# Kernel optimization log

Measured on AMD Instinct MI355X. Metric: run time of the kernel, lower is better.

The kernel has to match this reference:

```python
import jax, jax.numpy as jnp
import numpy as np
from jax import lax

K2 = 3                 # support_kernel_size
TARGET_OCC = 0.5
OCC_W = 10.0
ITERS = 10             # flood-fill iterations
THRESH = 0.5
STEEP = 20.0

# 6-neighbor 3D cross kernel (plus-shaped), shape [O=1, I=1, 3, 3, 3]
_cross_np = np.zeros((1, 1, 3, 3, 3), dtype=np.float32)
for dz, dy, dx in [(0, 1, 1), (2, 1, 1), (1, 0, 1), (1, 2, 1), (1, 1, 0), (1, 1, 2)]:
    _cross_np[0, 0, dz, dy, dx] = 1.0


def _conv3d(x, k, pad):
    # x: [B, C, D, H, W], k: [O, I, kd, kh, kw]
    return lax.conv_general_dilated(
        x, k, window_strides=(1, 1, 1), padding=pad,
        dimension_numbers=('NCDHW', 'OIDHW', 'NCDHW'))


def setup_inputs() -> dict:
    key = jax.random.key(0)
    voxel_grid = jax.random.uniform(key, (4, 1, 128, 128, 128), dtype=jnp.float32)
    return {"voxel_grid": voxel_grid}


def reference(voxel_grid):
    B, C, D, H, W = voxel_grid.shape
    N = B * D * H * W
    dt = voxel_grid.dtype

    # ---- overhang score: vectorized over all z-slices at once ----
    # per-slice conv2d(3x3 ones) == conv3d with kernel depth 1
    k2 = jnp.ones((1, 1, 1, K2, K2), dt)
    below = voxel_grid[:, :, :-1]          # [B,1,D-1,H,W]
    curr = voxel_grid[:, :, 1:]
    below_support = _conv3d(below, k2, ((0, 0), (1, 1), (1, 1)))
    support_ratio = below_support / (K2 * K2)
    overhang = (curr * (1.0 - support_ratio)).sum() / N

    # ---- surface area score ----
    k3 = jnp.ones((1, 1, 3, 3, 3), dt)
    neighbor_solid = _conv3d(voxel_grid, k3, ((1, 1), (1, 1), (1, 1)))
    surface_term = neighbor_solid.sum() / 27.0 / N

    occupancy = voxel_grid.sum() / N
    occupancy_penalty = OCC_W * (occupancy - TARGET_OCC) ** 2

    # differentiable flood-fill (diff_find_enclosed_voids)
    seed = jnp.zeros_like(voxel_grid).at[:, :, 5, 5, 5].set(1.0)
    cross = jnp.asarray(_cross_np, dt)
    not_solid = 1.0 - voxel_grid

    def body(i, mask):
        c = _conv3d(mask, cross, ((1, 1), (1, 1), (1, 1)))
        act = jax.nn.sigmoid(STEEP * (c - THRESH))
        return jnp.maximum(mask, act) * not_solid

    enclosed = lax.fori_loop(0, ITERS, body, seed)
    resin_trap_penalty = 100.0 * enclosed.sum() / N

    surface_score = surface_term - resin_trap_penalty - occupancy_penalty
    return overhang, surface_score
```

## Files before the change

### kernel.cpp

```cpp
#include <hip/hip_runtime.h>

#define HW    (128*128)
#define DHW   (128*128*128)
#define NTOT  (4*DHW)
#define NBLK  2048

__device__ __forceinline__ float sigf(float x){ return 1.0f/(1.0f+__expf(-x)); }
__device__ __forceinline__ float4 ld4(const float* p){ return *(const float4*)p; }


__global__ __launch_bounds__(256, 4) void mega_k(
    const float* __restrict__ v, float* __restrict__ p_occ,
    float* __restrict__ p_surf, float* __restrict__ p_over,
    float* __restrict__ p_trap)
{
    __shared__ float4 smem4[1445];
    __shared__ float sred[16];
    float* smem = (float*)smem4;

    const int bid = blockIdx.x;
    const int tid = threadIdx.x;
    const float4 zero4 = make_float4(0,0,0,0);

    if (bid < 4) {
        const int b = bid;
        const size_t gb = (size_t)b * DHW;
        const int ty = tid & 15, tz = tid >> 4;
        const float a_lo = sigf(-10.0f), a_hi = sigf(10.0f);
        #define M(zz,yy) (smem + (((zz)*17 + (yy))*20))

        float m[16], nv[16];
        {
            const float* rv = v + gb + ((size_t)tz*128 + ty)*128;
            int dzy = abs(tz-5) + abs(ty-5);
            #pragma unroll
            for (int q = 0; q < 4; ++q) {
                int x4 = 4*q;
                float4 a = ld4(rv + x4);
                nv[x4+0]=1.f-a.x; nv[x4+1]=1.f-a.y; nv[x4+2]=1.f-a.z; nv[x4+3]=1.f-a.w;
                int d0=dzy+abs(x4+0-5), d1=dzy+abs(x4+1-5);
                int d2=dzy+abs(x4+2-5), d3=dzy+abs(x4+3-5);
                m[x4+0] = ((d0==0)?1.f:((d0==1)?a_hi:a_lo)) * nv[x4+0];
                m[x4+1] = ((d1==0)?1.f:((d1==1)?a_hi:a_lo)) * nv[x4+1];
                m[x4+2] = ((d2==0)?1.f:((d2==1)?a_hi:a_lo)) * nv[x4+2];
                m[x4+3] = ((d3==0)?1.f:((d3==1)?a_hi:a_lo)) * nv[x4+3];
                *(float4*)(M(tz,ty) + x4) = make_float4(m[x4+0],m[x4+1],m[x4+2],m[x4+3]);
            }
        }
        const float xrE = a_lo * (1.f - v[gb + ((size_t)tz*128 + ty)*128 + 16]);
        {
            int a = tid >> 4, e = tid & 15;
            M(16,a)[e] = a_lo * (1.f - v[gb + ((size_t)16*128 + a)*128 + e]);
            M(a,16)[e] = a_lo * (1.f - v[gb + ((size_t)a*128 + 16)*128 + e]);
        }
        __syncthreads();

        for (int it = 0; it < 9; ++it) {
            const float* YM = M(tz,ty-1);
            const float* YP = M(tz,ty+1);
            const float* ZM = M(tz-1,ty);
            const float* ZP = M(tz+1,ty);
            float nm[16];
            #pragma unroll
            for (int q = 0; q < 4; ++q) {
                int x4 = 4*q;
                float4 ym = (ty > 0) ? *(const float4*)(YM + x4) : zero4;
                float4 yp = *(const float4*)(YP + x4);
                float4 zm = (tz > 0) ? *(const float4*)(ZM + x4) : zero4;
                float4 zp = *(const float4*)(ZP + x4);
                float xl = (q == 0) ? 0.f : m[x4-1];
                float xr = (q == 3) ? xrE : m[x4+4];
                float s0 = xl      + m[x4+1] + ym.x + yp.x + zm.x + zp.x;
                float s1 = m[x4+0] + m[x4+2] + ym.y + yp.y + zm.y + zp.y;
                float s2 = m[x4+1] + m[x4+3] + ym.z + yp.z + zm.z + zp.z;
                float s3 = m[x4+2] + xr      + ym.w + yp.w + zm.w + zp.w;
                nm[x4+0] = fmaxf(m[x4+0], sigf(20.f*s0 - 10.f)) * nv[x4+0];
                nm[x4+1] = fmaxf(m[x4+1], sigf(20.f*s1 - 10.f)) * nv[x4+1];
                nm[x4+2] = fmaxf(m[x4+2], sigf(20.f*s2 - 10.f)) * nv[x4+2];
                nm[x4+3] = fmaxf(m[x4+3], sigf(20.f*s3 - 10.f)) * nv[x4+3];
            }
            __syncthreads();
            float* W = M(tz,ty);
            #pragma unroll
            for (int q = 0; q < 4; ++q) {
                int x4 = 4*q;
                *(float4*)(W + x4) = make_float4(nm[x4+0],nm[x4+1],nm[x4+2],nm[x4+3]);
                m[x4+0]=nm[x4+0]; m[x4+1]=nm[x4+1]; m[x4+2]=nm[x4+2]; m[x4+3]=nm[x4+3];
            }
            __syncthreads();
        }

        float d = 0.f;
        #pragma unroll
        for (int x = 0; x < 16; ++x) d += m[x] - a_lo * nv[x];
        #pragma unroll
        for (int o = 32; o; o >>= 1) d += __shfl_down(d, o, 64);
        int lane = tid & 63, wid = tid >> 6;
        if (lane == 0) sred[wid] = d;
        __syncthreads();
        if (tid == 0) p_trap[b] = sred[0] + sred[1] + sred[2] + sred[3];
        #undef M
    } else {
        const int rid = bid - 4;
        const int b   = rid >> 9;
        const int rem = rid & 511;
        const int z0  = (rem >> 4) * 4;
        const int y0  = (rem & 15) * 8;
        const int tx  = tid & 31, ty = tid >> 5;
        const int x4  = tx * 4;
        const int y   = y0 + ty;
        const size_t gb = (size_t)b * DHW;
        #define PB(p,r) (smem + ((p)*1320 + (r)*132))

        float occ = 0.f, surf = 0.f, over = 0.f;

        if (z0 >= 1) {
            const float* bp = v + gb + (size_t)(z0-1)*HW;
            for (int i = tid; i < 320; i += 256) {
                int r = i >> 5, xq = i & 31, xi = xq*4;
                int gy = y0 - 1 + r;
                float4 q = ((unsigned)gy <= 127u) ? ld4(bp + gy*128 + xi) : zero4;
                float ql = __shfl_up(q.w, 1);   if (xq == 0)  ql = 0.f;
                float qr = __shfl_down(q.x, 1); if (xq == 31) qr = 0.f;
                *(float4*)(PB(0,r) + xi) =
                    make_float4(ql+q.x+q.y, q.x+q.y+q.z, q.y+q.z+q.w, q.z+q.w+qr);
            }
        }
        __syncthreads();

        const float wy = (y==0 || y==127) ? 2.f : 3.f;
        const float wx0 = (x4==0)   ? 2.f : 3.f;
        const float wx3 = (x4==124) ? 2.f : 3.f;
        const float inv9 = 1.f/9.f;

        int pb = 0;
        for (int s = 0; s < 4; ++s) {
            const int z = z0 + s;
            const float* cp = v + gb + (size_t)z*HW;
            float4 val = ld4(cp + y*128 + x4);

            occ += val.x + val.y + val.z + val.w;
            float wz = (z==0 || z==127) ? 2.f : 3.f;
            surf += wz*wy*(wx0*val.x + 3.f*val.y + 3.f*val.z + wx3*val.w);

            if (z >= 1) {
                float4 a = *(const float4*)(PB(pb, ty)   + x4);
                float4 c = *(const float4*)(PB(pb, ty+1) + x4);
                float4 d = *(const float4*)(PB(pb, ty+2) + x4);
                float4 S = make_float4(a.x+c.x+d.x, a.y+c.y+d.y,
                                       a.z+c.z+d.z, a.w+c.w+d.w);
                over += val.x*(1.f - S.x*inv9) + val.y*(1.f - S.y*inv9)
                      + val.z*(1.f - S.z*inv9) + val.w*(1.f - S.w*inv9);
            }

            if (s < 3) {
                float ql = __shfl_up(val.w, 1);   if (tx == 0)  ql = 0.f;
                float qr = __shfl_down(val.x, 1); if (tx == 31) qr = 0.f;
                *(float4*)(PB(pb^1, ty+1) + x4) =
                    make_float4(ql+val.x+val.y, val.x+val.y+val.z,
                                val.y+val.z+val.w, val.z+val.w+qr);
                if (tid < 64) {
                    int h = tid >> 5, xq = tid & 31, xi = xq*4;
                    int gy = h ? (y0 + 8) : (y0 - 1);
                    float4 q = ((unsigned)gy <= 127u) ? ld4(cp + gy*128 + xi) : zero4;
                    float hl = __shfl_up(q.w, 1);   if (xq == 0)  hl = 0.f;
                    float hr = __shfl_down(q.x, 1); if (xq == 31) hr = 0.f;
                    *(float4*)(PB(pb^1, h*9) + xi) =
                        make_float4(hl+q.x+q.y, q.x+q.y+q.z, q.y+q.z+q.w, q.z+q.w+hr);
                }
                pb ^= 1;
            }
            __syncthreads();
        }

        #pragma unroll
        for (int o = 32; o; o >>= 1) {
            occ  += __shfl_down(occ,  o, 64);
            surf += __shfl_down(surf, o, 64);
            over += __shfl_down(over, o, 64);
        }
        int lane = tid & 63, wid = tid >> 6;
        if (lane == 0) { sred[wid]=occ; sred[4+wid]=surf; sred[8+wid]=over; }
        __syncthreads();
        if (tid == 0) {
            p_occ [rid] = sred[0]+sred[1]+sred[2]+sred[3];
            p_surf[rid] = sred[4]+sred[5]+sred[6]+sred[7];
            p_over[rid] = sred[8]+sred[9]+sred[10]+sred[11];
        }
        #undef PB
    }
}

__global__ __launch_bounds__(1024) void finalize_k(
    const float* __restrict__ p_occ, const float* __restrict__ p_surf,
    const float* __restrict__ p_over, const float* __restrict__ p_trap,
    float* __restrict__ out)
{
    double occ=0, surf=0, over=0;
    for (int i = threadIdx.x; i < NBLK; i += 1024) {
        occ += p_occ[i]; surf += p_surf[i]; over += p_over[i];
    }
    __shared__ double sm[3][16];
    #pragma unroll
    for (int o = 32; o; o >>= 1) {
        occ  += __shfl_down(occ,  o, 64);
        surf += __shfl_down(surf, o, 64);
        over += __shfl_down(over, o, 64);
    }
    int lane = threadIdx.x & 63, wid = threadIdx.x >> 6;
    if (lane == 0) { sm[0][wid]=occ; sm[1][wid]=surf; sm[2][wid]=over; }
    __syncthreads();
    if (threadIdx.x == 0) {
        double so=0, ss=0, sv=0;
        for (int w = 0; w < 16; ++w) { so+=sm[0][w]; ss+=sm[1][w]; sv+=sm[2][w]; }
        double dS = (double)p_trap[0] + p_trap[1] + p_trap[2] + p_trap[3];
        double a_lo = 1.0 / (1.0 + exp(10.0));
        double N = (double)NTOT;
        double trap_sum = a_lo * (N - so) + dS;
        double occupancy = so / N;
        double occ_pen = 10.0 * (occupancy - 0.5) * (occupancy - 0.5);
        out[0] = (float)(sv / N);
        out[1] = (float)(ss / 27.0 / N - 100.0 * trap_sum / N - occ_pen);
    }
}

extern "C" void kernel_launch(void* const* d_in, const int* in_sizes, int n_in,
                              void* d_out, int out_size, void* d_ws, size_t ws_size,
                              hipStream_t stream)
{
    const float* v = (const float*)d_in[0];
    float* out = (float*)d_out;
    float* ws = (float*)d_ws;

    float* p_occ  = ws;
    float* p_surf = p_occ  + NBLK;
    float* p_over = p_surf + NBLK;
    float* p_trap = p_over + NBLK;

    mega_k<<<NBLK + 4, 256, 0, stream>>>(v, p_occ, p_surf, p_over, p_trap);
    finalize_k<<<1, 1024, 0, stream>>>(p_occ, p_surf, p_over, p_trap, out);
}
```

Before: 85.61 us.

## Register-tile the stencil blocks over z and drop shared-memory double buffering

The streaming statistics blocks now give each thread one z-slice and eight y-rows. The current and below-slice rows are loaded straight into registers, and the 3-wide x sums are built with lane shuffles. This removes the shared-memory ping-pong buffers and the per-slice __syncthreads, and halves the number of blocks, since each block now covers 8 z-slices. In exchange, each thread re-reads the below-slice halo rows that were previously shared across z steps, which adds global/L2 traffic and register pressure.

```diff
diff --git a/kernel.cpp b/kernel.cpp
--- a/kernel.cpp
+++ b/kernel.cpp
@@ -3,7 +3,7 @@
 #define HW    (128*128)
 #define DHW   (128*128*128)
 #define NTOT  (4*DHW)
-#define NBLK  2048
+#define NBLK  1024
 
 __device__ __forceinline__ float sigf(float x){ return 1.0f/(1.0f+__expf(-x)); }
 __device__ __forceinline__ float4 ld4(const float* p){ return *(const float4*)p; }
@@ -102,75 +102,62 @@
         #undef M
     } else {
         const int rid = bid - 4;
-        const int b   = rid >> 9;
-        const int rem = rid & 511;
-        const int z0  = (rem >> 4) * 4;
+        const int b   = rid >> 8;
+        const int rem = rid & 255;
+        const int z0  = (rem >> 4) * 8;
         const int y0  = (rem & 15) * 8;
-        const int tx  = tid & 31, ty = tid >> 5;
+        const int tx  = tid & 31;
+        const int tz  = tid >> 5;
+        const int z   = z0 + tz;
         const int x4  = tx * 4;
-        const int y   = y0 + ty;
         const size_t gb = (size_t)b * DHW;
-        #define PB(p,r) (smem + ((p)*1320 + (r)*132))
+        const float* cp = v + gb + (size_t)z * HW;
+        const float* bp = cp - HW;
 
         float occ = 0.f, surf = 0.f, over = 0.f;
 
-        if (z0 >= 1) {
-            const float* bp = v + gb + (size_t)(z0-1)*HW;
-            for (int i = tid; i < 320; i += 256) {
-                int r = i >> 5, xq = i & 31, xi = xq*4;
+        float4 qb[10];
+        if (z >= 1) {
+            #pragma unroll
+            for (int r = 0; r < 10; ++r) {
                 int gy = y0 - 1 + r;
-                float4 q = ((unsigned)gy <= 127u) ? ld4(bp + gy*128 + xi) : zero4;
-                float ql = __shfl_up(q.w, 1);   if (xq == 0)  ql = 0.f;
-                float qr = __shfl_down(q.x, 1); if (xq == 31) qr = 0.f;
-                *(float4*)(PB(0,r) + xi) =
-                    make_float4(ql+q.x+q.y, q.x+q.y+q.z, q.y+q.z+q.w, q.z+q.w+qr);
-            }
-        }
-        __syncthreads();
-
-        const float wy = (y==0 || y==127) ? 2.f : 3.f;
+                qb[r] = ((unsigned)gy <= 127u) ? ld4(bp + gy*128 + x4) : zero4;
+            }
+        }
+        float4 qc[8];
+        #pragma unroll
+        for (int i = 0; i < 8; ++i) qc[i] = ld4(cp + (y0+i)*128 + x4);
+
+        float4 P[10];
+        if (z >= 1) {
+            #pragma unroll
+            for (int r = 0; r < 10; ++r) {
+                float4 q = qb[r];
+                float ql = __shfl_up(q.w, 1);   if (tx == 0)  ql = 0.f;
+                float qr = __shfl_down(q.x, 1); if (tx == 31) qr = 0.f;
+                P[r] = make_float4(ql+q.x+q.y, q.x+q.y+q.z,
+                                   q.y+q.z+q.w, q.z+q.w+qr);
+            }
+        }
+
+        const float wz  = (z==0 || z==127) ? 2.f : 3.f;
         const float wx0 = (x4==0)   ? 2.f : 3.f;
         const float wx3 = (x4==124) ? 2.f : 3.f;
         const float inv9 = 1.f/9.f;
-
-        int pb = 0;
-        for (int s = 0; s < 4; ++s) {
-            const int z = z0 + s;
-            const float* cp = v + gb + (size_t)z*HW;
-            float4 val = ld4(cp + y*128 + x4);
-
+        #pragma unroll
+        for (int i = 0; i < 8; ++i) {
+            const int y = y0 + i;
+            float4 val = qc[i];
             occ += val.x + val.y + val.z + val.w;
-            float wz = (z==0 || z==127) ? 2.f : 3.f;
+            float wy = (y==0 || y==127) ? 2.f : 3.f;
             surf += wz*wy*(wx0*val.x + 3.f*val.y + 3.f*val.z + wx3*val.w);
-
             if (z >= 1) {
-                float4 a = *(const float4*)(PB(pb, ty)   + x4);
-                float4 c = *(const float4*)(PB(pb, ty+1) + x4);
-                float4 d = *(const float4*)(PB(pb, ty+2) + x4);
+                float4 a = P[i], c = P[i+1], d = P[i+2];
                 float4 S = make_float4(a.x+c.x+d.x, a.y+c.y+d.y,
                                        a.z+c.z+d.z, a.w+c.w+d.w);
                 over += val.x*(1.f - S.x*inv9) + val.y*(1.f - S.y*inv9)
                       + val.z*(1.f - S.z*inv9) + val.w*(1.f - S.w*inv9);
             }
-
-            if (s < 3) {
-                float ql = __shfl_up(val.w, 1);   if (tx == 0)  ql = 0.f;
-                float qr = __shfl_down(val.x, 1); if (tx == 31) qr = 0.f;
-                *(float4*)(PB(pb^1, ty+1) + x4) =
-                    make_float4(ql+val.x+val.y, val.x+val.y+val.z,
-                                val.y+val.z+val.w, val.z+val.w+qr);
-                if (tid < 64) {
-                    int h = tid >> 5, xq = tid & 31, xi = xq*4;
-                    int gy = h ? (y0 + 8) : (y0 - 1);
-                    float4 q = ((unsigned)gy <= 127u) ? ld4(cp + gy*128 + xi) : zero4;
-                    float hl = __shfl_up(q.w, 1);   if (xq == 0)  hl = 0.f;
-                    float hr = __shfl_down(q.x, 1); if (xq == 31) hr = 0.f;
-                    *(float4*)(PB(pb^1, h*9) + xi) =
-                        make_float4(hl+q.x+q.y, q.x+q.y+q.z, q.y+q.z+q.w, q.z+q.w+hr);
-                }
-                pb ^= 1;
-            }
-            __syncthreads();
         }
 
         #pragma unroll
@@ -187,7 +174,6 @@
             p_surf[rid] = sred[4]+sred[5]+sred[6]+sred[7];
             p_over[rid] = sred[8]+sred[9]+sred[10]+sred[11];
         }
-        #undef PB
     }
 }
 
```

Result: faster. 83.43 us (-2.5%).
